# Kernel optimization log

Measured on AMD Instinct MI355X. Metric: run time of the kernel, lower is better.

## Reference

```python
import jax, jax.numpy as jnp
import numpy as np

VOCAB, D, N, K, L = 6144, 1024, 4, 8, 3
D_FF, N_STREAMS, SINK_ITERS = 3072, 4, 20
ALPHA = 4.0      # surrogate sigmoid sharpness
EK_FLOOR = 0.0
B, S = 4, 128

@jax.custom_vjp
def spike(x):
    return (x >= 0.).astype(x.dtype)

def _spike_fwd(x):
    return (x >= 0.).astype(x.dtype), x

def _spike_bwd(x, g):
    s = jax.nn.sigmoid(ALPHA * x)
    return (g * ALPHA * s * (1. - s),)

spike.defvjp(_spike_fwd, _spike_bwd)

def plif_scan(beta, x, v_th):
    # PLIF recurrence over leading time axis. x: (T,B,C); beta, v_th: (C,).
    # v_t = beta*v + (1-beta)*x_t ; heaviside spike (sigmoid surrogate); soft reset.
    # Returns spike current v_th * spike (matches spike_current_activation).
    def step(v, x_t):
        v = beta * v + (1. - beta) * x_t
        s = spike(v - v_th)
        return v - v_th * s, v_th * s
    v0 = jnp.zeros(x.shape[1:], x.dtype)
    _, cur = jax.lax.scan(step, v0, x)
    return cur

def sinkhorn(logits):
    # doubly-stochastic projection (Birkhoff polytope), fixed iteration count
    M = jnp.exp(logits)
    for _ in range(SINK_ITERS):
        M = M / M.sum(1, keepdims=True)
        M = M / M.sum(0, keepdims=True)
    return M

def rmsnorm(x, w, eps=1e-6):
    return x * w * jax.lax.rsqrt(jnp.mean(x * x, axis=-1, keepdims=True) + eps)

def lateral_inhibition(x, w, eps=1e-6):
    xc = x - x.mean(axis=-1, keepdims=True)
    return w * xc * jax.lax.rsqrt(jnp.mean(xc * xc, axis=-1, keepdims=True) + eps)

LAYER_KEYS = ['H_logits','w_pre','w_post','beta_in1','vth_in1','W_in','beta_h','vth_h','W_out','beta_in2','vth_in2','W_gate','beta_gate','vth_gate','W_up','beta_up','vth_up','W_down','halt_w','halt_b']

def layer_forward(h, p):
    # h: (S, B, n, D) multi-stream residual
    Sq, Bq = h.shape[0], h.shape[1]
    H = sinkhorn(p['H_logits'])                                   # (n,n) doubly stochastic
    h_mix = jnp.einsum('mn,sbnd->sbmd', H, h)                     # mHC stream mixing
    x = jnp.einsum('n,sbnd->sbd', jax.nn.softmax(p['w_pre']), h_mix)
    x_tk = jnp.repeat(x, K, axis=0)                               # (S*K, B, D) K-frame unroll
    s1 = plif_scan(p['beta_in1'], x_tk, p['vth_in1'])             # input_neuron1
    sh = plif_scan(p['beta_h'], s1 @ p['W_in'], p['vth_h'])       # snn_block hidden (N*D)
    y_blk = sh @ p['W_out']                                       # (TK,B,D)
    s2 = plif_scan(p['beta_in2'], x_tk + y_blk, p['vth_in2'])     # input_neuron2
    g = plif_scan(p['beta_gate'], s2 @ p['W_gate'], p['vth_gate'])  # snn_ffn gate
    u = plif_scan(p['beta_up'], s2 @ p['W_up'], p['vth_up'])        # snn_ffn up
    y = y_blk + (g * u) @ p['W_down']                             # (TK,B,D)
    yk = y.reshape(Sq, K, Bq, D)
    # PonderNet halting over the K frames of each token
    lam = jax.nn.sigmoid(jnp.einsum('skbd,d->skb', yk, p['halt_w']) + p['halt_b'])
    keep = jnp.cumprod(1. - lam, axis=1)
    prev = jnp.concatenate([jnp.ones_like(keep[:, :1]), keep[:, :-1]], axis=1)
    pk = lam * prev
    pk = pk.at[:, -1].add(1. - pk.sum(axis=1))                    # remainder to last frame
    y_tok = jnp.einsum('skb,skbd->sbd', pk, yk)
    ek = jnp.einsum('skb,k->sb', pk, jnp.arange(1, K + 1, dtype=y.dtype)).mean()
    efc = jnp.maximum(EK_FLOOR - ek, 0.)
    w_post = jax.nn.softmax(p['w_post'])
    h_out = h_mix + w_post[None, None, :, None] * y_tok[:, :, None, :]
    return h_out, ek, efc

def _forward(token_ids, embed, norm_w, decode_W, decode_b, out_norm_w, beta_out, vth_out, stacked):
    emb = embed[token_ids]                                        # (B,S,D)
    h = jnp.transpose(emb, (1, 0, 2))[:, :, None, :]
    h = jnp.broadcast_to(h, (emb.shape[1], emb.shape[0], N_STREAMS, D))  # (S,B,n,D)
    pcs, efcs = [], []
    for l in range(L):
        p = {k: stacked[k][l] for k in LAYER_KEYS}
        h, pc, efc = layer_forward(h, p)
        pcs.append(pc); efcs.append(efc)
    ponder = sum(pcs) / L
    ekf = sum(efcs) / L
    # decode: collapse streams -> K-frame output neuron -> tied embedding logits
    h_coll = h.mean(axis=2)                                       # (S,B,D)
    h_tk = jnp.repeat(h_coll, K, axis=0)                          # (S*K,B,D)
    h_tk = rmsnorm(h_tk, out_norm_w)
    cur = plif_scan(beta_out, h_tk, vth_out)
    decoded = cur.reshape(h_coll.shape[0], K, h_coll.shape[1], D).mean(axis=1)
    decoded = jnp.transpose(decoded, (1, 0, 2))                   # (B,S,D)
    hh = decoded @ decode_W.T + decode_b
    hh = lateral_inhibition(hh, norm_w)
    logits = hh @ embed.T                                         # tied embedding
    return logits, ponder, ekf

def setup_inputs() -> dict:
    key = jax.random.key(0)
    ks = iter(jax.random.split(key, 48))
    def nrm(shape, std):
        return jax.random.normal(next(ks), shape, jnp.float32) * std
    def beta_init(shape):
        return 0.4 + 0.4 * jax.random.uniform(next(ks), shape, jnp.float32)
    def vth_init(shape):
        return 0.1 + 0.3 * jax.random.uniform(next(ks), shape, jnp.float32)
    inp = dict(
        token_ids=jax.random.randint(next(ks), (B, S), 0, VOCAB),
        embed=nrm((VOCAB, D), 0.02),
        norm_w=jnp.ones((D,), jnp.float32),
        decode_W=nrm((D, D), 1. / np.sqrt(D)),
        decode_b=jnp.zeros((D,), jnp.float32),
        out_norm_w=jnp.ones((D,), jnp.float32),
        beta_out=beta_init((D,)), vth_out=vth_init((D,)),
        H_logits=nrm((L, N_STREAMS, N_STREAMS), 0.1),
        w_pre=nrm((L, N_STREAMS), 0.1),
        w_post=nrm((L, N_STREAMS), 0.1),
        beta_in1=beta_init((L, D)), vth_in1=vth_init((L, D)),
        W_in=nrm((L, D, N * D), 1. / np.sqrt(D)),
        beta_h=beta_init((L, N * D)), vth_h=vth_init((L, N * D)),
        W_out=nrm((L, N * D, D), 1. / np.sqrt(N * D)),
        beta_in2=beta_init((L, D)), vth_in2=vth_init((L, D)),
        W_gate=nrm((L, D, D_FF), 1. / np.sqrt(D)),
        beta_gate=beta_init((L, D_FF)), vth_gate=vth_init((L, D_FF)),
        W_up=nrm((L, D, D_FF), 1. / np.sqrt(D)),
        beta_up=beta_init((L, D_FF)), vth_up=vth_init((L, D_FF)),
        W_down=nrm((L, D_FF, D), 1. / np.sqrt(D_FF)),
        halt_w=nrm((L, D), 0.02),
        halt_b=jnp.full((L,), 1.0, jnp.float32),
    )
    return inp

def reference(token_ids, embed, norm_w, decode_W, decode_b, out_norm_w, beta_out, vth_out, H_logits, w_pre, w_post, beta_in1, vth_in1, W_in, beta_h, vth_h, W_out, beta_in2, vth_in2, W_gate, beta_gate, vth_gate, W_up, beta_up, vth_up, W_down, halt_w, halt_b):
    stacked = dict(H_logits=H_logits, w_pre=w_pre, w_post=w_post, beta_in1=beta_in1, vth_in1=vth_in1, W_in=W_in, beta_h=beta_h, vth_h=vth_h, W_out=W_out, beta_in2=beta_in2, vth_in2=vth_in2, W_gate=W_gate, beta_gate=beta_gate, vth_gate=vth_gate, W_up=W_up, beta_up=beta_up, vth_up=vth_up, W_down=W_down, halt_w=halt_w, halt_b=halt_b)
    return _forward(token_ids, embed, norm_w, decode_W, decode_b, out_norm_w, beta_out, vth_out, stacked)
```

## Files before the change

kernel.cpp:

```cpp
#include <hip/hip_runtime.h>
#include <hip/hip_bf16.h>

#define B 4
#define S 128
#define D 1024
#define NS 4
#define KF 8
#define LNUM 3
#define DFF 3072
#define ND 4096
#define T 1024
#define TB 4096
#define VOCABSZ 6144
#define SINKIT 20

typedef unsigned short u16;
typedef __attribute__((ext_vector_type(8))) short short8;
typedef __attribute__((ext_vector_type(4))) float f32x4;

__device__ __forceinline__ void gload16(const void* g, void* l) {
  __builtin_amdgcn_global_load_lds(
      (const __attribute__((address_space(1))) void*)g,
      (__attribute__((address_space(3))) void*)l, 16, 0, 0);
}

__global__ void sink_kernel(const float* __restrict__ Hl, const float* __restrict__ wpre,
                            const float* __restrict__ wpost, float* __restrict__ prm) {
  if (threadIdx.x != 0 || blockIdx.x != 0) return;
  float M[16];
  for (int i = 0; i < 16; ++i) M[i] = expf(Hl[i]);
  for (int it = 0; it < SINKIT; ++it) {
    for (int m = 0; m < 4; ++m) {
      float s = M[m*4+0] + M[m*4+1] + M[m*4+2] + M[m*4+3];
      for (int n = 0; n < 4; ++n) M[m*4+n] /= s;
    }
    for (int n = 0; n < 4; ++n) {
      float s = M[0*4+n] + M[1*4+n] + M[2*4+n] + M[3*4+n];
      for (int m = 0; m < 4; ++m) M[m*4+n] /= s;
    }
  }
  for (int i = 0; i < 16; ++i) prm[i] = M[i];
  float a[4], mx, sm;
  mx = fmaxf(fmaxf(wpre[0], wpre[1]), fmaxf(wpre[2], wpre[3]));
  sm = 0.f; for (int i = 0; i < 4; ++i) { a[i] = expf(wpre[i] - mx); sm += a[i]; }
  for (int i = 0; i < 4; ++i) prm[16+i] = a[i] / sm;
  mx = fmaxf(fmaxf(wpost[0], wpost[1]), fmaxf(wpost[2], wpost[3]));
  sm = 0.f; for (int i = 0; i < 4; ++i) { a[i] = expf(wpost[i] - mx); sm += a[i]; }
  for (int i = 0; i < 4; ++i) prm[20+i] = a[i] / sm;
}

__global__ __launch_bounds__(256)
void gather_kernel(const int* __restrict__ tok, const float* __restrict__ embed,
                   float* __restrict__ h) {
  const int idx = blockIdx.x * 256 + threadIdx.x;
  const int d   = idx % D;
  const int sbn = idx / D;
  const int sb  = sbn / NS;
  const int b   = sb % B, s = sb / B;
  h[idx] = embed[(size_t)tok[b*S + s] * D + d];
}

__global__ __launch_bounds__(256)
void mix_kernel(const float* __restrict__ h, const float* __restrict__ P,
                float* __restrict__ h_mix, float* __restrict__ x) {
  const int idx = blockIdx.x * 256 + threadIdx.x;
  const int d = idx % D, sb = idx / D;
  const float* hp = h + (size_t)sb * NS * D + d;
  const float h0 = hp[0], h1 = hp[D], h2 = hp[2*D], h3 = hp[3*D];
  float xv = 0.f;
  #pragma unroll
  for (int m = 0; m < 4; ++m) {
    float hm = P[m*4+0]*h0 + P[m*4+1]*h1 + P[m*4+2]*h2 + P[m*4+3]*h3;
    h_mix[(size_t)sb * NS * D + m*D + d] = hm;
    xv = fmaf(P[16+m], hm, xv);
  }
  x[idx] = xv;
}

template<bool R1, bool A2>
__global__ __launch_bounds__(256)
void plif_kernel(const float* __restrict__ z1, const float* __restrict__ z2,
                 const float* __restrict__ beta, const float* __restrict__ vth,
                 u16* __restrict__ outp, int C) {
  const int idx = blockIdx.x * 256 + threadIdx.x;
  const int c = idx % C;
  const int stride = B * C;
  const float be = beta[c], vt = vth[c], omb = 1.f - be;
  float v = 0.f;
  constexpr int PF = 32;
  float xA[PF], yA[PF], xB[PF], yB[PF];

#define PLOAD(xa, ya, tb) do {                                               \
    if (R1) {                                                                \
      _Pragma("unroll")                                                      \
      for (int i = 0; i < PF/8; ++i)                                         \
        xa[i] = z1[(size_t)((tb)/8 + i) * stride + idx];                     \
    } else {                                                                 \
      _Pragma("unroll")                                                      \
      for (int i = 0; i < PF; ++i)                                           \
        xa[i] = z1[(size_t)((tb) + i) * stride + idx];                       \
    }                                                                        \
    if (A2) {                                                                \
      _Pragma("unroll")                                                      \
      for (int i = 0; i < PF; ++i)                                           \
        ya[i] = z2[(size_t)((tb) + i) * stride + idx];                       \
    }                                                                        \
  } while (0)

#define PCOMP(xa, ya, tb) do {                                               \
    _Pragma("unroll")                                                        \
    for (int i = 0; i < PF; ++i) {                                           \
      float xt = R1 ? xa[i >> 3] : xa[i];                                    \
      if (A2) xt += ya[i];                                                   \
      v = fmaf(be, v, omb * xt);                                             \
      const bool sp = (v >= vt);                                             \
      if (sp) v -= vt;                                                       \
      outp[(size_t)((tb) + i) * stride + idx] = sp ? (u16)0x3F80 : (u16)0;   \
    }                                                                        \
  } while (0)

  PLOAD(xA, yA, 0);
  for (int tb = 0; tb < T; tb += 2*PF) {
    PLOAD(xB, yB, tb + PF);
    PCOMP(xA, yA, tb);
    if (tb + 2*PF < T) PLOAD(xA, yA, tb + 2*PF);
    PCOMP(xB, yB, tb + PF);
  }
#undef PLOAD
#undef PCOMP
}

__global__ __launch_bounds__(256)
void plif_gu_kernel(const float* __restrict__ z12,
                    const float* __restrict__ bg, const float* __restrict__ vg_,
                    const float* __restrict__ bu, const float* __restrict__ vu_,
                    u16* __restrict__ outp) {
  const int idx = blockIdx.x * 256 + threadIdx.x;
  const int c = idx % DFF, b = idx / DFF;
  const float beg = bg[c], vtg = vg_[c], beu = bu[c], vtu = vu_[c];
  const float og = 1.f - beg, ou = 1.f - beu;
  float vg = 0.f, vu = 0.f;
  constexpr int PF = 32;
  float gA[PF], uA[PF], gB[PF], uB[PF];

#define GLOAD_(ga, ua, tb) do {                                              \
    _Pragma("unroll")                                                        \
    for (int i = 0; i < PF; ++i) {                                           \
      const size_t off_ = ((size_t)((tb) + i) * B + b) * (2*DFF) + c;        \
      ga[i] = z12[off_];                                                     \
      ua[i] = z12[off_ + DFF];                                               \
    }                                                                        \
  } while (0)

#define GCOMP_(ga, ua, tb) do {                                              \
    _Pragma("unroll")                                                        \
    for (int i = 0; i < PF; ++i) {                                           \
      vg = fmaf(beg, vg, og * ga[i]);                                        \
      vu = fmaf(beu, vu, ou * ua[i]);                                        \
      const bool sg = (vg >= vtg), su = (vu >= vtu);                         \
      if (sg) vg -= vtg;                                                     \
      if (su) vu -= vtu;                                                     \
      outp[(size_t)((tb) + i) * (B*DFF) + idx] = (sg && su) ? (u16)0x3F80 : (u16)0; \
    }                                                                        \
  } while (0)

  GLOAD_(gA, uA, 0);
  for (int tb = 0; tb < T; tb += 2*PF) {
    GLOAD_(gB, uB, tb + PF);
    GCOMP_(gA, uA, tb);
    if (tb + 2*PF < T) GLOAD_(gA, uA, tb + 2*PF);
    GCOMP_(gB, uB, tb + PF);
  }
#undef GLOAD_
#undef GCOMP_
}

__global__ __launch_bounds__(256)
void prep_t_kernel(const float* __restrict__ W, const float* __restrict__ sA,
                   const float* __restrict__ sB, float mult,
                   u16* __restrict__ wt, int Kd, int Nd) {
  __shared__ float tile[64][65];
  const int tid = threadIdx.x;
  const int bn = blockIdx.x, bk = blockIdx.y;
  const int c = tid & 63, r0 = (tid >> 6) * 16;
  #pragma unroll
  for (int i = 0; i < 16; ++i) {
    const int r = r0 + i;
    const int kg = bk*64 + r;
    float s = mult;
    if (sA) s *= sA[kg];
    if (sB) s *= sB[kg];
    tile[r][c] = W[(size_t)kg * Nd + bn*64 + c] * s;
  }
  __syncthreads();
  const int K2 = 2 * Kd;
  #pragma unroll
  for (int i = 0; i < 16; ++i) {
    const int nl = r0 + i;
    const float v = tile[c][nl];
    const __hip_bfloat16 h = __float2bfloat16(v);
    const size_t off = (size_t)(bn*64 + nl) * K2 + bk*64 + c;
    wt[off] = *(const u16*)&h;
    const __hip_bfloat16 lo = __float2bfloat16(v - __bfloat162float(h));
    wt[off + Kd] = *(const u16*)&lo;
  }
}

__global__ __launch_bounds__(256)
void prep_nt_kernel(const float* __restrict__ W, const float* __restrict__ sK, float mult,
                    u16* __restrict__ wt, int Kd) {
  const size_t idx = (size_t)blockIdx.x * 256 + threadIdx.x;
  const int k = (int)(idx % Kd);
  const size_t n = idx / Kd;
  const float v = W[idx] * mult * (sK ? sK[k] : 1.f);
  const __hip_bfloat16 h = __float2bfloat16(v);
  const size_t off = n * (2*Kd) + k;
  wt[off] = *(const u16*)&h;
  const __hip_bfloat16 lo = __float2bfloat16(v - __bfloat162float(h));
  wt[off + Kd] = *(const u16*)&lo;
}


template<bool ADDC>
__global__ __launch_bounds__(256)
void mgemm2_kernel(const u16* __restrict__ A, const u16* __restrict__ Bm,
                   const float* __restrict__ Cin, float* __restrict__ Cout,
                   int M, int N, int Astride, int AW, int BW, int Bstride, int K2) {
  __shared__ __align__(16) char lds[49152];
  const int tid = threadIdx.x;
  const int lane = tid & 63, wv = tid >> 6;
  const int wm = wv >> 1, wn = wv & 1;
  const int lr = lane & 15, ks = lane >> 4;
  const int rs3 = (lr >> 1) & 3;

  const int gx = gridDim.x;
  const int nwg = gx * gridDim.y;
  int flat = blockIdx.y * gx + blockIdx.x;
  flat = (flat & 7) * (nwg >> 3) + (flat >> 3);
  const int bn = flat % gx, bm = flat / gx;

  f32x4 acc[4][4];
  #pragma unroll
  for (int i = 0; i < 4; ++i)
    #pragma unroll
    for (int j = 0; j < 4; ++j) acc[i][j] = (f32x4){0.f, 0.f, 0.f, 0.f};

  const size_t am0 = (size_t)bm * 128, bn0 = (size_t)bn * 128;

#define STAGE(bufbase, k0) do {                                                  \
    const int aoff_ = ((k0) >= AW) ? (k0) - AW : (k0);                           \
    const int boff_ = ((k0) >= BW) ? (k0) - BW : (k0);                           \
    _Pragma("unroll")                                                            \
    for (int c_ = 0; c_ < 2; ++c_) {                                             \
      const int bo_ = c_*4096 + wv*1024 + lane*16;                               \
      const int row_ = bo_ >> 6;                                                 \
      const int csrc_ = ((bo_ >> 4) & 3) ^ ((row_ >> 1) & 3);                    \
      gload16((const char*)A + ((am0 + row_) * (size_t)Astride + aoff_ + csrc_*8) * 2, \
              lds + (bufbase) + c_*4096 + wv*1024);                              \
      gload16((const char*)Bm + ((bn0 + row_) * (size_t)Bstride + boff_ + csrc_*8) * 2, \
              lds + (bufbase) + 8192 + c_*4096 + wv*1024);                       \
    }                                                                            \
  } while (0)

  const int nt = K2 >> 5;
  STAGE(0, 0);
  if (nt > 1) STAGE(16384, 32);
  int bc = 0;
  for (int t = 0; t < nt; ++t) {
    if (t + 2 < nt) {
      int bs = bc + 2; if (bs >= 3) bs -= 3;
      STAGE(bs * 16384, (t + 2) << 5);
      asm volatile("s_waitcnt vmcnt(8)\n\ts_barrier" ::: "memory");
    } else if (t + 1 < nt) {
      asm volatile("s_waitcnt vmcnt(4)\n\ts_barrier" ::: "memory");
    } else {
      asm volatile("s_waitcnt vmcnt(0)\n\ts_barrier" ::: "memory");
    }
    const char* la = lds + bc * 16384;
    const char* lb = la + 8192;
    short8 af[4], bf[4];
    #pragma unroll
    for (int f = 0; f < 4; ++f) {
      af[f] = *(const short8*)(la + (wm*64 + f*16 + lr)*64 + ((ks ^ rs3) * 16));
      bf[f] = *(const short8*)(lb + (wn*64 + f*16 + lr)*64 + ((ks ^ rs3) * 16));
    }
    #pragma unroll
    for (int i = 0; i < 4; ++i)
      #pragma unroll
      for (int j = 0; j < 4; ++j)
        acc[i][j] = __builtin_amdgcn_mfma_f32_16x16x32_bf16(af[i], bf[j], acc[i][j], 0, 0, 0);
    asm volatile("s_barrier" ::: "memory");
    bc = bc + 1; if (bc >= 3) bc = 0;
  }
#undef STAGE

  const int col0 = bn*128 + wn*64 + lr;
  #pragma unroll
  for (int i = 0; i < 4; ++i)
    #pragma unroll
    for (int j = 0; j < 4; ++j) {
      const size_t rbase = (size_t)(bm*128 + wm*64 + i*16 + ks*4);
      #pragma unroll
      for (int r = 0; r < 4; ++r) {
        const size_t idx = (rbase + r) * (size_t)N + col0 + j*16;
        float v = acc[i][j][r];
        if (ADDC) v += Cin[idx];
        Cout[idx] = v;
      }
    }
}

__global__ __launch_bounds__(512)
void mgemm3_kernel(const u16* __restrict__ A, const u16* __restrict__ Bm,
                   float* __restrict__ Cout, int M, int N, int Astride, int AW, int K2) {
  __shared__ __align__(16) char lds[131072];
  const int tid = threadIdx.x;
  const int lane = tid & 63, wv = tid >> 6;
  const int wm = wv >> 2, wn = wv & 3;
  const int lr = lane & 15, ks = lane >> 4;
  const int rs3 = (lr >> 1) & 3;

  const int gx = gridDim.x;
  const int nwg = gx * gridDim.y;
  int flat = blockIdx.y * gx + blockIdx.x;
  flat = (flat & 7) * (nwg >> 3) + (flat >> 3);
  const int bn = flat % gx, bm = flat / gx;

  f32x4 acc[2][2][4][2];
  #pragma unroll
  for (int a0 = 0; a0 < 2; ++a0)
    #pragma unroll
    for (int a1 = 0; a1 < 2; ++a1)
      #pragma unroll
      for (int a2 = 0; a2 < 4; ++a2)
        #pragma unroll
        for (int a3 = 0; a3 < 2; ++a3)
          acc[a0][a1][a2][a3] = (f32x4){0.f, 0.f, 0.f, 0.f};

  const size_t am0 = (size_t)bm * 256, bn0 = (size_t)bn * 256;
  short8 af[2][4];
  short8 bf[2][2][2];

#define STG_U(ISB, TILE, HALF) do {                                               \
    const int tk_ = (TILE) * 64;                                                  \
    const int aof_ = (ISB) ? tk_ : ((tk_ >= AW) ? tk_ - AW : tk_);                \
    _Pragma("unroll")                                                             \
    for (int kk_ = 0; kk_ < 2; ++kk_) {                                           \
      const int fl_ = wv*1024 + lane*16;                                          \
      const int row_ = (HALF)*128 + (fl_ >> 6);                                   \
      const int csrc_ = ((fl_ >> 4) & 3) ^ ((row_ >> 1) & 3);                     \
      const u16* gp_ = (ISB)                                                      \
        ? (Bm + (bn0 + row_) * (size_t)K2 + tk_ + kk_*32 + csrc_*8)               \
        : (A  + (am0 + row_) * (size_t)Astride + aof_ + kk_*32 + csrc_*8);        \
      gload16(gp_, lds + ((ISB)?65536:0) + ((TILE)&1)*32768 + kk_*16384 + fl_ + (HALF)*8192); \
    }                                                                             \
  } while (0)

#define PHASE(D_, IH, JH, RA, RB, SISB, STILE, SHALF, SVALID) do {                \
    if (lastit) asm volatile("s_waitcnt vmcnt(0)" ::: "memory");                  \
    else        asm volatile("s_waitcnt vmcnt(6)" ::: "memory");                  \
    if (RA) {                                                                     \
      _Pragma("unroll")                                                           \
      for (int kk = 0; kk < 2; ++kk)                                              \
        _Pragma("unroll")                                                         \
        for (int i = 0; i < 4; ++i)                                               \
          af[kk][i] = *(const short8*)(lds + (D_)*32768 + kk*16384 +              \
              ((IH)*128 + wm*64 + i*16 + lr)*64 + ((ks ^ rs3)*16));               \
    }                                                                             \
    if (RB) {                                                                     \
      _Pragma("unroll")                                                           \
      for (int kk = 0; kk < 2; ++kk)                                              \
        _Pragma("unroll")                                                         \
        for (int j = 0; j < 2; ++j)                                               \
          bf[JH][kk][j] = *(const short8*)(lds + 65536 + (D_)*32768 + kk*16384 +  \
              ((JH)*128 + wn*32 + j*16 + lr)*64 + ((ks ^ rs3)*16));               \
    }                                                                             \
    if (SVALID) STG_U(SISB, STILE, SHALF);                                        \
    asm volatile("s_barrier" ::: "memory");                                       \
    asm volatile("s_waitcnt lgkmcnt(0)" ::: "memory");                            \
    __builtin_amdgcn_sched_barrier(0);                                            \
    __builtin_amdgcn_s_setprio(1);                                                \
    _Pragma("unroll")                                                             \
    for (int i = 0; i < 4; ++i)                                                   \
      _Pragma("unroll")                                                           \
      for (int j = 0; j < 2; ++j)                                                 \
        _Pragma("unroll")                                                         \
        for (int kk = 0; kk < 2; ++kk)                                            \
          acc[IH][JH][i][j] = __builtin_amdgcn_mfma_f32_16x16x32_bf16(            \
              af[kk][i], bf[JH][kk][j], acc[IH][JH][i][j], 0, 0, 0);              \
    __builtin_amdgcn_s_setprio(0);                                                \
    asm volatile("s_barrier" ::: "memory");                                       \
  } while (0)

  const int nt2 = K2 >> 6;
  const int niter = nt2 >> 1;
  STG_U(0, 0, 0); STG_U(1, 0, 0); STG_U(0, 0, 1); STG_U(1, 0, 1);
  STG_U(0, 1, 0); STG_U(1, 1, 0);

  for (int t = 0; t < niter; ++t) {
    const int t1 = 2*t + 1, t2 = 2*t + 2, t3 = 2*t + 3;
    const bool s2 = (t2 < nt2), s3 = (t3 < nt2);
    const bool lastit = (t + 1 >= niter);
    PHASE(0, 0, 0, 1, 1, 0, t1, 1, true);
    PHASE(0, 0, 1, 0, 1, 1, t1, 1, true);
    PHASE(0, 1, 0, 1, 0, 0, t2, 0, s2);
    PHASE(0, 1, 1, 0, 0, 1, t2, 0, s2);
    PHASE(1, 0, 0, 1, 1, 0, t2, 1, s2);
    PHASE(1, 0, 1, 0, 1, 1, t2, 1, s2);
    PHASE(1, 1, 0, 1, 0, 0, t3, 0, s3);
    PHASE(1, 1, 1, 0, 0, 1, t3, 0, s3);
  }
#undef PHASE
#undef STG_U

  #pragma unroll
  for (int ih = 0; ih < 2; ++ih)
    #pragma unroll
    for (int jh = 0; jh < 2; ++jh) {
      const int col0 = bn*256 + jh*128 + wn*32 + lr;
      #pragma unroll
      for (int i = 0; i < 4; ++i)
        #pragma unroll
        for (int j = 0; j < 2; ++j) {
          const size_t rbase = (size_t)(bm*256 + ih*128 + wm*64 + i*16 + ks*4);
          #pragma unroll
          for (int r = 0; r < 4; ++r)
            Cout[(rbase + r) * (size_t)N + col0 + j*16] = acc[ih][jh][i][j][r];
        }
    }
}

__global__ __launch_bounds__(256)
void halt_kernel(const float* __restrict__ y, const float* __restrict__ h_mix,
                 const float* __restrict__ P, const float* __restrict__ hw,
                 const float* __restrict__ hb, float* __restrict__ h_out,
                 float* __restrict__ ek_acc) {
  const int sb = blockIdx.x;
  const int b = sb % B, s = sb / B;
  const int tid = threadIdx.x;
  __shared__ float red[256];
  __shared__ float lam_s[KF];
  __shared__ float pk_s[KF];

  for (int k = 0; k < KF; ++k) {
    const float* yr = y + ((size_t)(s*KF + k) * B + b) * D;
    float p = 0.f;
    for (int d = tid; d < D; d += 256) p = fmaf(yr[d], hw[d], p);
    red[tid] = p; __syncthreads();
    for (int off = 128; off > 0; off >>= 1) {
      if (tid < off) red[tid] += red[tid + off];
      __syncthreads();
    }
    if (tid == 0) lam_s[k] = 1.f / (1.f + expf(-(red[0] + hb[0])));
    __syncthreads();
  }
  if (tid == 0) {
    float keep = 1.f, sum = 0.f, pk[KF];
    #pragma unroll
    for (int k = 0; k < KF; ++k) { pk[k] = lam_s[k] * keep; keep *= (1.f - lam_s[k]); sum += pk[k]; }
    pk[KF-1] += 1.f - sum;
    float ek = 0.f;
    #pragma unroll
    for (int k = 0; k < KF; ++k) { ek += pk[k] * (float)(k + 1); pk_s[k] = pk[k]; }
    atomicAdd(ek_acc, ek);
  }
  __syncthreads();
  for (int d = tid; d < D; d += 256) {
    float yt = 0.f;
    #pragma unroll
    for (int k = 0; k < KF; ++k)
      yt = fmaf(pk_s[k], y[((size_t)(s*KF + k) * B + b) * D + d], yt);
    #pragma unroll
    for (int n = 0; n < NS; ++n) {
      const size_t off = ((size_t)sb * NS + n) * D + d;
      h_out[off] = h_mix[off] + P[20+n] * yt;
    }
  }
}

__global__ __launch_bounds__(256)
void collnorm_kernel(const float* __restrict__ h, const float* __restrict__ w,
                     float* __restrict__ xn) {
  const int sb = blockIdx.x, tid = threadIdx.x;
  __shared__ float red[256];
  float vals[4]; float ss = 0.f;
  #pragma unroll
  for (int i = 0; i < 4; ++i) {
    const int d = tid + i*256;
    const float* hp = h + (size_t)sb * NS * D + d;
    float m = 0.25f * (hp[0] + hp[D] + hp[2*D] + hp[3*D]);
    vals[i] = m; ss += m*m;
  }
  red[tid] = ss; __syncthreads();
  for (int off = 128; off > 0; off >>= 1) { if (tid < off) red[tid] += red[tid + off]; __syncthreads(); }
  const float inv = 1.f / sqrtf(red[0] * (1.f/(float)D) + 1e-6f);
  #pragma unroll
  for (int i = 0; i < 4; ++i) {
    const int d = tid + i*256;
    xn[(size_t)sb * D + d] = vals[i] * w[d] * inv;
  }
}

__global__ __launch_bounds__(256)
void dplif_kernel(const float* __restrict__ xn, const float* __restrict__ beta,
                  const float* __restrict__ vth, u16* __restrict__ dec) {
  const int idx = blockIdx.x * 256 + threadIdx.x;
  const int b = idx / D, d = idx % D;
  const float be = beta[d], vt = vth[d], omb = 1.f - be;
  float v = 0.f;
  for (int s = 0; s < S; ++s) {
    const float xv = xn[((size_t)s * B + b) * D + d];
    float cnt = 0.f;
    #pragma unroll
    for (int k = 0; k < KF; ++k) {
      v = fmaf(be, v, omb * xv);
      if (v >= vt) { v -= vt; cnt += 1.f; }
    }
    const __hip_bfloat16 hb_ = __float2bfloat16(cnt);
    dec[((size_t)b * S + s) * D + d] = *(const u16*)&hb_;
  }
}

__global__ __launch_bounds__(256)
void li_kernel(float* __restrict__ hh, const float* __restrict__ bias,
               const float* __restrict__ w) {
  const int r = blockIdx.x, tid = threadIdx.x;
  __shared__ float red[256];
  float* row = hh + (size_t)r * D;
  float v[4]; float sm = 0.f;
  #pragma unroll
  for (int i = 0; i < 4; ++i) { const int d = tid + i*256; v[i] = row[d] + bias[d]; sm += v[i]; }
  red[tid] = sm; __syncthreads();
  for (int off = 128; off > 0; off >>= 1) { if (tid < off) red[tid] += red[tid + off]; __syncthreads(); }
  const float mean = red[0] * (1.f/(float)D);
  __syncthreads();
  float ss = 0.f;
  #pragma unroll
  for (int i = 0; i < 4; ++i) { v[i] -= mean; ss += v[i]*v[i]; }
  red[tid] = ss; __syncthreads();
  for (int off = 128; off > 0; off >>= 1) { if (tid < off) red[tid] += red[tid + off]; __syncthreads(); }
  const float inv = 1.f / sqrtf(red[0] * (1.f/(float)D) + 1e-6f);
  #pragma unroll
  for (int i = 0; i < 4; ++i) { const int d = tid + i*256; row[d] = w[d] * v[i] * inv; }
}

__global__ __launch_bounds__(256)
void split_kernel(const float* __restrict__ X, u16* __restrict__ xs, int Kd) {
  const size_t idx = (size_t)blockIdx.x * 256 + threadIdx.x;
  const int k = (int)(idx % Kd);
  const size_t n = idx / Kd;
  const float v = X[idx];
  const __hip_bfloat16 h = __float2bfloat16(v);
  const size_t off = n * (2*Kd) + k;
  xs[off] = *(const u16*)&h;
  const __hip_bfloat16 lo = __float2bfloat16(v - __bfloat162float(h));
  xs[off + Kd] = *(const u16*)&lo;
}

__global__ void finalize_kernel(const float* __restrict__ ek_acc, float* __restrict__ tail) {
  if (threadIdx.x != 0 || blockIdx.x != 0) return;
  float ponder = 0.f, ekf = 0.f;
  for (int l = 0; l < LNUM; ++l) {
    float ek = ek_acc[l] * (1.f/(float)(S*B));
    ponder += ek;
    ekf += fmaxf(0.f - ek, 0.f);
  }
  tail[0] = ponder * (1.f/(float)LNUM);
  tail[1] = ekf * (1.f/(float)LNUM);
}

extern "C" void kernel_launch(void* const* d_in, const int* in_sizes, int n_in,
                              void* d_out, int out_size, void* d_ws, size_t ws_size,
                              hipStream_t stream) {
  const int*   tok       = (const int*)  d_in[0];
  const float* embed     = (const float*)d_in[1];
  const float* norm_w    = (const float*)d_in[2];
  const float* decode_W  = (const float*)d_in[3];
  const float* decode_b  = (const float*)d_in[4];
  const float* out_norm  = (const float*)d_in[5];
  const float* beta_out  = (const float*)d_in[6];
  const float* vth_out   = (const float*)d_in[7];
  const float* H_logits  = (const float*)d_in[8];
  const float* w_pre     = (const float*)d_in[9];
  const float* w_post    = (const float*)d_in[10];
  const float* beta_in1  = (const float*)d_in[11];
  const float* vth_in1   = (const float*)d_in[12];
  const float* W_in      = (const float*)d_in[13];
  const float* beta_h    = (const float*)d_in[14];
  const float* vth_h     = (const float*)d_in[15];
  const float* W_out     = (const float*)d_in[16];
  const float* beta_in2  = (const float*)d_in[17];
  const float* vth_in2   = (const float*)d_in[18];
  const float* W_gate    = (const float*)d_in[19];
  const float* beta_gate = (const float*)d_in[20];
  const float* vth_gate  = (const float*)d_in[21];
  const float* W_up      = (const float*)d_in[22];
  const float* beta_up   = (const float*)d_in[23];
  const float* vth_up    = (const float*)d_in[24];
  const float* W_down    = (const float*)d_in[25];
  const float* halt_w    = (const float*)d_in[26];
  const float* halt_b    = (const float*)d_in[27];
  float* out = (float*)d_out;

  float* ws = (float*)d_ws;
  size_t o = 0;
  float* prm   = ws + o; o += 256;
  float* h_cur = ws + o; o += (size_t)S*B*NS*D;
  float* h_mix = ws + o; o += (size_t)S*B*NS*D;
  float* xbuf  = ws + o; o += (size_t)S*B*D;
  float* y_blk = ws + o; o += (size_t)TB*D;
  float* zbig  = ws + o; o += (size_t)TB*2*DFF;
  u16*   spb   = (u16*)(ws + o); o += (size_t)TB*ND/2;
  u16*   s1b   = (u16*)(ws + o); o += (size_t)TB*D/2;
  u16*   s2b   = (u16*)(ws + o); o += (size_t)TB*D/2;
  float* xn    = ws + o; o += (size_t)S*B*D;
  u16*   decb  = (u16*)(ws + o); o += (size_t)B*S*D/2;
  float* hh    = ws + o; o += (size_t)B*S*D;
  u16*   wt    = (u16*)(ws + o); o += (size_t)(2*DFF)*D;
  if (ws_size < o * sizeof(float)) return;

  float* ek_acc = prm + 96;
  hipMemsetAsync(ek_acc, 0, 3 * sizeof(float), stream);

  gather_kernel<<<(S*B*NS*D)/256, 256, 0, stream>>>(tok, embed, h_cur);

  for (int l = 0; l < LNUM; ++l) {
    float* P = prm + l*32;
    sink_kernel<<<1, 64, 0, stream>>>(H_logits + l*16, w_pre + l*4, w_post + l*4, P);
    mix_kernel<<<(S*B*D)/256, 256, 0, stream>>>(h_cur, P, h_mix, xbuf);
    plif_kernel<true,false><<<(B*D)/256, 256, 0, stream>>>(
        xbuf, nullptr, beta_in1 + l*D, vth_in1 + l*D, s1b, D);

    { dim3 gp(ND/64, D/64);
      prep_t_kernel<<<gp, 256, 0, stream>>>(W_in + (size_t)l*D*ND, vth_in1 + l*D, nullptr, 1.f,
                                            wt, D, ND); }
    { dim3 g(ND/256, TB/256);
      mgemm3_kernel<<<g, 512, 0, stream>>>(s1b, wt, zbig, TB, ND, D, D, 2*D); }
    plif_kernel<false,false><<<(B*ND)/256, 256, 0, stream>>>(
        zbig, nullptr, beta_h + l*ND, vth_h + l*ND, spb, ND);

    { dim3 gp(D/64, ND/64);
      prep_t_kernel<<<gp, 256, 0, stream>>>(W_out + (size_t)l*ND*D, vth_h + l*ND, nullptr, 1.f,
                                            wt, ND, D); }
    { dim3 g(D/128, TB/128);
      mgemm2_kernel<false><<<g, 256, 0, stream>>>(spb, wt, nullptr, y_blk, TB, D,
                                                  ND, ND, 2*ND, 2*ND, 2*ND); }
    plif_kernel<true,true><<<(B*D)/256, 256, 0, stream>>>(
        xbuf, y_blk, beta_in2 + l*D, vth_in2 + l*D, s2b, D);

    { dim3 gp(DFF/64, D/64);
      prep_t_kernel<<<gp, 256, 0, stream>>>(W_gate + (size_t)l*D*DFF, vth_in2 + l*D, nullptr, 1.f,
                                            wt, D, DFF);
      prep_t_kernel<<<gp, 256, 0, stream>>>(W_up + (size_t)l*D*DFF, vth_in2 + l*D, nullptr, 1.f,
                                            wt + (size_t)DFF*2*D, D, DFF); }
    { dim3 g((2*DFF)/256, TB/256);
      mgemm3_kernel<<<g, 512, 0, stream>>>(s2b, wt, zbig, TB, 2*DFF, D, D, 2*D); }
    plif_gu_kernel<<<(B*DFF)/256, 256, 0, stream>>>(
        zbig, beta_gate + l*DFF, vth_gate + l*DFF, beta_up + l*DFF, vth_up + l*DFF, spb);

    { dim3 gp(D/64, DFF/64);
      prep_t_kernel<<<gp, 256, 0, stream>>>(W_down + (size_t)l*DFF*D, vth_gate + l*DFF,
                                            vth_up + l*DFF, 1.f, wt, DFF, D); }
    { dim3 g(D/128, TB/128);
      mgemm2_kernel<true><<<g, 256, 0, stream>>>(spb, wt, y_blk, y_blk, TB, D,
                                                 DFF, DFF, 2*DFF, 2*DFF, 2*DFF); }
    halt_kernel<<<S*B, 256, 0, stream>>>(y_blk, h_mix, P, halt_w + l*D, halt_b + l, h_cur, ek_acc + l);
  }

  collnorm_kernel<<<S*B, 256, 0, stream>>>(h_cur, out_norm, xn);
  dplif_kernel<<<(B*D)/256, 256, 0, stream>>>(xn, beta_out, vth_out, decb);

  prep_nt_kernel<<<(D*D)/256, 256, 0, stream>>>(decode_W, vth_out, 0.125f, wt, D);
  { dim3 g(D/128, (B*S)/128);
    mgemm2_kernel<false><<<g, 256, 0, stream>>>(decb, wt, nullptr, hh, B*S, D,
                                                D, D, 2*D, 2*D, 2*D); }
  li_kernel<<<B*S, 256, 0, stream>>>(hh, decode_b, norm_w);

  u16* hh_c  = (u16*)(zbig + 6600000);
  u16* emb_c = (u16*)zbig;
  split_kernel<<<(B*S*D)/256, 256, 0, stream>>>(hh, hh_c, D);
  prep_nt_kernel<<<(VOCABSZ*D)/256, 256, 0, stream>>>(embed, nullptr, 1.f, emb_c, D);
  { dim3 g(VOCABSZ/128, (B*S)/128);
    mgemm2_kernel<false><<<g, 256, 0, stream>>>(hh_c, emb_c, nullptr, out, B*S, VOCABSZ,
                                                2*D, D, 2*D, 2*D, 3*D); }
  finalize_kernel<<<1, 1, 0, stream>>>(ek_acc, out + (out_size - 2));
}
```

Measured before the change: 2.071 ms.

## Split-K the narrow W_out and W_down GEMMs with 256-tile kernel plus reduction

The N=1024 output GEMMs (W_out with K=2*ND, W_down with K=2*DFF) move from the 128x128 mgemm2 kernel to the 256x256 mgemm3 kernel, split four ways along K via blockIdx.z. Partial results go to scratch and a new vectorized reduce4 kernel sums them, adding the residual where needed. The aim is better CU occupancy and tile efficiency for these GEMMs, which otherwise launch only 64 large tiles. The cost is extra partial-sum traffic through memory and an additional kernel launch per GEMM.

```diff
diff --git a/kernel.cpp b/kernel.cpp
--- a/kernel.cpp
+++ b/kernel.cpp
@@ -220,6 +220,26 @@
   wt[off + Kd] = *(const u16*)&lo;
 }
 
+template<bool ADDC>
+__global__ __launch_bounds__(256)
+void reduce4_kernel(float* __restrict__ out, const float* __restrict__ p, size_t n) {
+  const size_t i = ((size_t)blockIdx.x * 256 + threadIdx.x) * 4;
+  float4 a = *(const float4*)(p + i);
+  float4 b = *(const float4*)(p + n + i);
+  float4 c = *(const float4*)(p + 2*n + i);
+  float4 d = *(const float4*)(p + 3*n + i);
+  float4 o;
+  o.x = (a.x + b.x) + (c.x + d.x);
+  o.y = (a.y + b.y) + (c.y + d.y);
+  o.z = (a.z + b.z) + (c.z + d.z);
+  o.w = (a.w + b.w) + (c.w + d.w);
+  if (ADDC) {
+    const float4 e = *(const float4*)(out + i);
+    o.x += e.x; o.y += e.y; o.z += e.z; o.w += e.w;
+  }
+  *(float4*)(out + i) = o;
+}
+
 
 template<bool ADDC>
 __global__ __launch_bounds__(256)
@@ -312,7 +332,8 @@
 
 __global__ __launch_bounds__(512)
 void mgemm3_kernel(const u16* __restrict__ A, const u16* __restrict__ Bm,
-                   float* __restrict__ Cout, int M, int N, int Astride, int AW, int K2) {
+                   float* __restrict__ Cout, int M, int N, int Astride, int AW,
+                   int Bstride, int KC) {
   __shared__ __align__(16) char lds[131072];
   const int tid = threadIdx.x;
   const int lane = tid & 63, wv = tid >> 6;
@@ -325,6 +346,8 @@
   int flat = blockIdx.y * gx + blockIdx.x;
   flat = (flat & 7) * (nwg >> 3) + (flat >> 3);
   const int bn = flat % gx, bm = flat / gx;
+  const int k0base = blockIdx.z * KC;
+  Cout += (size_t)blockIdx.z * ((size_t)M * N);
 
   f32x4 acc[2][2][4][2];
   #pragma unroll
@@ -342,7 +365,7 @@
   short8 bf[2][2][2];
 
 #define STG_U(ISB, TILE, HALF) do {                                               \
-    const int tk_ = (TILE) * 64;                                                  \
+    const int tk_ = k0base + (TILE) * 64;                                         \
     const int aof_ = (ISB) ? tk_ : ((tk_ >= AW) ? tk_ - AW : tk_);                \
     _Pragma("unroll")                                                             \
     for (int kk_ = 0; kk_ < 2; ++kk_) {                                           \
@@ -350,7 +373,7 @@
       const int row_ = (HALF)*128 + (fl_ >> 6);                                   \
       const int csrc_ = ((fl_ >> 4) & 3) ^ ((row_ >> 1) & 3);                     \
       const u16* gp_ = (ISB)                                                      \
-        ? (Bm + (bn0 + row_) * (size_t)K2 + tk_ + kk_*32 + csrc_*8)               \
+        ? (Bm + (bn0 + row_) * (size_t)Bstride + tk_ + kk_*32 + csrc_*8)          \
         : (A  + (am0 + row_) * (size_t)Astride + aof_ + kk_*32 + csrc_*8);        \
       gload16(gp_, lds + ((ISB)?65536:0) + ((TILE)&1)*32768 + kk_*16384 + fl_ + (HALF)*8192); \
     }                                                                             \
@@ -392,7 +415,7 @@
     asm volatile("s_barrier" ::: "memory");                                       \
   } while (0)
 
-  const int nt2 = K2 >> 6;
+  const int nt2 = KC >> 6;
   const int niter = nt2 >> 1;
   STG_U(0, 0, 0); STG_U(1, 0, 0); STG_U(0, 0, 1); STG_U(1, 0, 1);
   STG_U(0, 1, 0); STG_U(1, 1, 0);
@@ -634,17 +657,17 @@
     { dim3 gp(ND/64, D/64);
       prep_t_kernel<<<gp, 256, 0, stream>>>(W_in + (size_t)l*D*ND, vth_in1 + l*D, nullptr, 1.f,
                                             wt, D, ND); }
-    { dim3 g(ND/256, TB/256);
-      mgemm3_kernel<<<g, 512, 0, stream>>>(s1b, wt, zbig, TB, ND, D, D, 2*D); }
+    { dim3 g(ND/256, TB/256, 1);
+      mgemm3_kernel<<<g, 512, 0, stream>>>(s1b, wt, zbig, TB, ND, D, D, 2*D, 2*D); }
     plif_kernel<false,false><<<(B*ND)/256, 256, 0, stream>>>(
         zbig, nullptr, beta_h + l*ND, vth_h + l*ND, spb, ND);
 
     { dim3 gp(D/64, ND/64);
       prep_t_kernel<<<gp, 256, 0, stream>>>(W_out + (size_t)l*ND*D, vth_h + l*ND, nullptr, 1.f,
                                             wt, ND, D); }
-    { dim3 g(D/128, TB/128);
-      mgemm2_kernel<false><<<g, 256, 0, stream>>>(spb, wt, nullptr, y_blk, TB, D,
-                                                  ND, ND, 2*ND, 2*ND, 2*ND); }
+    { dim3 g(D/256, TB/256, 4);
+      mgemm3_kernel<<<g, 512, 0, stream>>>(spb, wt, zbig, TB, D, ND, ND, 2*ND, 2048); }
+    reduce4_kernel<false><<<(TB*D)/1024, 256, 0, stream>>>(y_blk, zbig, (size_t)TB*D);
     plif_kernel<true,true><<<(B*D)/256, 256, 0, stream>>>(
         xbuf, y_blk, beta_in2 + l*D, vth_in2 + l*D, s2b, D);
 
@@ -653,17 +676,17 @@
                                             wt, D, DFF);
       prep_t_kernel<<<gp, 256, 0, stream>>>(W_up + (size_t)l*D*DFF, vth_in2 + l*D, nullptr, 1.f,
                                             wt + (size_t)DFF*2*D, D, DFF); }
-    { dim3 g((2*DFF)/256, TB/256);
-      mgemm3_kernel<<<g, 512, 0, stream>>>(s2b, wt, zbig, TB, 2*DFF, D, D, 2*D); }
+    { dim3 g((2*DFF)/256, TB/256, 1);
+      mgemm3_kernel<<<g, 512, 0, stream>>>(s2b, wt, zbig, TB, 2*DFF, D, D, 2*D, 2*D); }
     plif_gu_kernel<<<(B*DFF)/256, 256, 0, stream>>>(
         zbig, beta_gate + l*DFF, vth_gate + l*DFF, beta_up + l*DFF, vth_up + l*DFF, spb);
 
     { dim3 gp(D/64, DFF/64);
       prep_t_kernel<<<gp, 256, 0, stream>>>(W_down + (size_t)l*DFF*D, vth_gate + l*DFF,
                                             vth_up + l*DFF, 1.f, wt, DFF, D); }
-    { dim3 g(D/128, TB/128);
-      mgemm2_kernel<true><<<g, 256, 0, stream>>>(spb, wt, y_blk, y_blk, TB, D,
-                                                 DFF, DFF, 2*DFF, 2*DFF, 2*DFF); }
+    { dim3 g(D/256, TB/256, 4);
+      mgemm3_kernel<<<g, 512, 0, stream>>>(spb, wt, zbig, TB, D, DFF, DFF, 2*DFF, 1536); }
+    reduce4_kernel<true><<<(TB*D)/1024, 256, 0, stream>>>(y_blk, zbig, (size_t)TB*D);
     halt_kernel<<<S*B, 256, 0, stream>>>(y_blk, h_mix, P, halt_w + l*D, halt_b + l, h_cur, ek_acc + l);
   }
 
```

Measured after the change: 1.959 ms, median of 2. -5.4%, faster.
